# Optimization experiments

Hardware: AMD Instinct MI355X
Metric: run time of the kernel (lower is better)

## Reference

```python
import jax, jax.numpy as jnp
from jax import lax
import numpy as np

EPS = 1e-8
NUM_ROUTES = 1152  # 32 * 6 * 6
NUM_OBJ = 10
OBJ_DIM = 16
PC_CAPS = 8
PC_CH = 32


def _squash(s, axis=-1):
    sq = jnp.sum(s * s, axis=axis, keepdims=True)
    return (sq / (1.0 + sq)) * s / jnp.sqrt(sq + EPS)


def setup_inputs() -> dict:
    key = jax.random.key(0)
    ks = jax.random.split(key, 12)
    B = 512
    image = jax.random.uniform(ks[0], (B, 1, 28, 28), dtype=jnp.float32)
    label = jax.random.randint(ks[1], (B,), 0, NUM_OBJ)
    conv_w = jax.random.normal(ks[2], (256, 1, 9, 9), dtype=jnp.float32) * 0.05
    conv_b = jnp.zeros((256,), jnp.float32)
    pc_w = jax.random.normal(ks[3], (PC_CAPS, PC_CH, 256, 9, 9), dtype=jnp.float32) * 0.02
    pc_b = jnp.zeros((PC_CAPS, PC_CH), jnp.float32)
    W_route = jax.random.normal(ks[4], (NUM_ROUTES, NUM_OBJ, OBJ_DIM, PC_CAPS), dtype=jnp.float32)
    dec_w1 = jax.random.normal(ks[5], (512, NUM_OBJ * OBJ_DIM), dtype=jnp.float32) * 0.05
    dec_b1 = jnp.zeros((512,), jnp.float32)
    dec_w2 = jax.random.normal(ks[6], (1024, 512), dtype=jnp.float32) * 0.05
    dec_b2 = jnp.zeros((1024,), jnp.float32)
    dec_w3 = jax.random.normal(ks[7], (784, 1024), dtype=jnp.float32) * 0.05
    dec_b3 = jnp.zeros((784,), jnp.float32)
    return {"image": image, "label": label, "conv_w": conv_w, "conv_b": conv_b,
            "pc_w": pc_w, "pc_b": pc_b, "W_route": W_route,
            "dec_w1": dec_w1, "dec_b1": dec_b1, "dec_w2": dec_w2, "dec_b2": dec_b2,
            "dec_w3": dec_w3, "dec_b3": dec_b3}


def reference(image, label, conv_w, conv_b, pc_w, pc_b, W_route,
              dec_w1, dec_b1, dec_w2, dec_b2, dec_w3, dec_b3):
    B = image.shape[0]
    # ConvEncoder: [B,1,28,28] -> [B,256,20,20]
    x = lax.conv_general_dilated(image, conv_w, (1, 1), 'VALID',
                                 dimension_numbers=('NCHW', 'OIHW', 'NCHW'))
    x = jax.nn.relu(x + conv_b[None, :, None, None])
    # PrimaryCaps: 8 parallel convs fused into one conv with 8*32 out channels
    pw = pc_w.reshape(PC_CAPS * PC_CH, 256, 9, 9)
    u = lax.conv_general_dilated(x, pw, (2, 2), 'VALID',
                                 dimension_numbers=('NCHW', 'OIHW', 'NCHW'))
    u = u + pc_b.reshape(-1)[None, :, None, None]  # [B,256,6,6] == stack dim=1 of [B,8,32,6,6]
    # faithful torch .view: [B,8,32,6,6] row-major -> [B,1152,8]
    u = u.reshape(B, NUM_ROUTES, PC_CAPS)
    u = _squash(u, axis=-1)
    # ObjectCaps dynamic routing
    # u_hat[b,r,j,o] = sum_c W[r,j,o,c] * u[b,r,c]
    u_hat = jnp.einsum('rjoc,brc->brjo', W_route, u)  # [B,1152,10,16]
    b_ij = jnp.zeros((B, NUM_ROUTES, NUM_OBJ), u_hat.dtype)
    v = None
    for it in range(3):
        c_ij = jax.nn.softmax(b_ij, axis=2)                  # softmax over capsules j
        s_j = jnp.einsum('brj,brjo->bjo', c_ij, u_hat)       # [B,10,16]
        v = _squash(s_j, axis=-1)
        if it < 2:
            b_ij = b_ij + jnp.einsum('brjo,bjo->brj', u_hat, v)
    obj_vectors = v[..., None]  # [B,10,16,1]
    # safe_norm over dim=2, squeeze(-1)
    y_prob = jnp.sqrt(jnp.sum(v * v, axis=-1) + EPS)  # [B,10]
    # Decoder: mask by label one-hot, MLP to reconstruction
    mask = jax.nn.one_hot(label, NUM_OBJ, dtype=v.dtype)
    masked = (v * mask[:, :, None]).reshape(B, NUM_OBJ * OBJ_DIM)
    h = jax.nn.relu(masked @ dec_w1.T + dec_b1)
    h = jax.nn.relu(h @ dec_w2.T + dec_b2)
    recon = jax.nn.sigmoid(h @ dec_w3.T + dec_b3).reshape(B, 1, 28, 28)
    return obj_vectors, recon, y_prob
```

## Files before the change

kernel.cpp:

```cpp
#include <hip/hip_runtime.h>
#include <hip/hip_bf16.h>

#define EPSF 1e-8f

typedef __attribute__((ext_vector_type(8))) short short8v;
typedef __attribute__((ext_vector_type(4))) float float4v;

static __device__ __forceinline__ unsigned short f2bf_bits(float x)
{
    return __builtin_bit_cast(unsigned short, __float2bfloat16(x));
}

__global__ __launch_bounds__(256) void k_bw2(const float* __restrict__ pw,
                                             __hip_bfloat16* __restrict__ Bw2)
{
    const int oc = blockIdx.x;
    const int t = threadIdx.x;
    __shared__ unsigned short wl[20736];
    for (int i = t; i < 20736; i += 256)
        wl[i] = f2bf_bits(pw[(size_t)oc * 20736 + i]);
    __syncthreads();
    const int r16 = oc & 15, nt = (oc >> 4) & 3, wcq = oc >> 6;
    for (int e = t; e < 2592; e += 256) {
        const int kidx = e >> 5, icc = (e >> 2) & 7, slot = e & 3;
        short8v v;
        #pragma unroll
        for (int i = 0; i < 8; ++i)
            v[i] = (short)wl[(icc * 32 + slot * 8 + i) * 81 + kidx];
        const int chunk = ((kidx * 8 + icc) * 4 + wcq) * 4 + nt;
        *(short8v*)(Bw2 + (size_t)chunk * 512 + (slot * 16 + r16) * 8) = v;
    }
}

__global__ __launch_bounds__(256) void k_conv1(const float* __restrict__ img,
                                               const float* __restrict__ cw,
                                               const float* __restrict__ cb,
                                               __hip_bfloat16* __restrict__ xt)
{
    const int b = blockIdx.x;
    const int c = threadIdx.x;
    __shared__ float simg[784];
    for (int i = c; i < 784; i += 256) simg[i] = img[b * 784 + i];
    float wreg[81];
    const float* wp = cw + c * 81;
    #pragma unroll
    for (int k = 0; k < 81; ++k) wreg[k] = wp[k];
    const float bias = cb[c];
    __syncthreads();

    const int icc = c >> 5, slot = (c >> 3) & 3, ic8 = c & 7;
    char* xbase = (char*)xt + ((size_t)b * 8 + icc) * 25600;

    for (int h = 0; h < 20; ++h) {
        for (int wg = 0; wg < 5; ++wg) {
            float acc[4] = {bias, bias, bias, bias};
            #pragma unroll
            for (int ky = 0; ky < 9; ++ky) {
                const float* rp = &simg[(h + ky) * 28 + wg * 4];
                float v[12];
                #pragma unroll
                for (int i = 0; i < 12; ++i) v[i] = rp[i];
                #pragma unroll
                for (int kx = 0; kx < 9; ++kx) {
                    const float wv = wreg[ky * 9 + kx];
                    #pragma unroll
                    for (int i = 0; i < 4; ++i)
                        acc[i] = fmaf(v[kx + i], wv, acc[i]);
                }
            }
            #pragma unroll
            for (int i = 0; i < 4; ++i) {
                int w = wg * 4 + i;
                float av = fmaxf(acc[i], 0.f);
                int pos = h * 20 + (w & 1) * 10 + (w >> 1);
                int off = pos * 64 + ((slot ^ ((pos >> 1) & 3)) << 4) + ic8 * 2;
                *(unsigned short*)(xbase + off) = f2bf_bits(av);
            }
        }
    }
}

__device__ __forceinline__ void stage_x(const __hip_bfloat16* __restrict__ xt,
                                        char* dst, int b0, int icc, int t)
{
    const __hip_bfloat16* base0 = xt + ((size_t)(b0    ) * 8 + icc) * 12800;
    const __hip_bfloat16* base1 = xt + ((size_t)(b0 + 1) * 8 + icc) * 12800;
    #pragma unroll
    for (int k = 0; k < 6; ++k) {
        const int unit = t + k * 512;
        const __hip_bfloat16* gp = (unit < 1600) ? (base0 + unit * 8)
                                                 : (base1 + (unit - 1600) * 8);
        __builtin_amdgcn_global_load_lds(
            (const __attribute__((address_space(1))) unsigned int*)gp,
            (__attribute__((address_space(3))) unsigned int*)(dst + unit * 16),
            16, 0, 0);
    }
    if (t < 128) {
        const int unit = 3072 + t;
        const __hip_bfloat16* gp = base1 + (unit - 1600) * 8;
        __builtin_amdgcn_global_load_lds(
            (const __attribute__((address_space(1))) unsigned int*)gp,
            (__attribute__((address_space(3))) unsigned int*)(dst + unit * 16),
            16, 0, 0);
    }
}

__global__ __launch_bounds__(512) void k_conv2(const __hip_bfloat16* __restrict__ xt,
                                               const __hip_bfloat16* __restrict__ Bw2,
                                               const float* __restrict__ pcb,
                                               float* __restrict__ u)
{
    const int b0 = blockIdx.x * 2;
    const int t = threadIdx.x;
    const int lane = t & 63, wid = t >> 6;
    const int wr = wid >> 2, wc = wid & 3;
    const int r16 = lane & 15, slot = lane >> 4;

    __shared__ alignas(16) char xs[2][51200];

    int lc[3];
    #pragma unroll
    for (int mt = 0; mt < 3; ++mt) {
        int hw = mt * 16 + r16;
        if (hw >= 36) hw = 0;
        int h = hw / 6, w = hw - h * 6;
        lc[mt] = 40 * h + w;
    }

    float4v acc[3][4];
    #pragma unroll
    for (int mt = 0; mt < 3; ++mt)
        #pragma unroll
        for (int nt = 0; nt < 4; ++nt)
            acc[mt][nt] = (float4v){0.f, 0.f, 0.f, 0.f};

    stage_x(xt, xs[0], b0, 0, t);
    __syncthreads();

    for (int icc = 0; icc < 8; ++icc) {
        const int cur = icc & 1;
        if (icc < 7) stage_x(xt, xs[cur ^ 1], b0, icc + 1, t);

        const char* xw = xs[cur] + wr * 25600;
        const size_t bK = ((size_t)icc * 4 + wc) * 2048 + lane * 8;

        #pragma unroll 3
        for (int kidx = 0; kidx < 81; ++kidx) {
            int ky = kidx / 9, kx = kidx - ky * 9;
            int scalK = 20 * ky + 10 * (kx & 1) + (kx >> 1);
            short8v a[3];
            #pragma unroll
            for (int mt = 0; mt < 3; ++mt) {
                int pos = lc[mt] + scalK;
                int off = pos * 64 + (((slot ^ (pos >> 1)) & 3) << 4);
                a[mt] = *(const short8v*)(xw + off);
            }
            const __hip_bfloat16* bp = Bw2 + (size_t)kidx * 65536 + bK;
            short8v bv[4];
            #pragma unroll
            for (int nt = 0; nt < 4; ++nt)
                bv[nt] = *(const short8v*)(bp + nt * 512);
            #pragma unroll
            for (int mt = 0; mt < 3; ++mt)
                #pragma unroll
                for (int nt = 0; nt < 4; ++nt)
                    acc[mt][nt] = __builtin_amdgcn_mfma_f32_16x16x32_bf16(a[mt], bv[nt], acc[mt][nt], 0, 0, 0);
        }
        __syncthreads();
    }

    const int b = b0 + wr;
    #pragma unroll
    for (int mt = 0; mt < 3; ++mt) {
        int hwb = mt * 16 + slot * 4;
        if (hwb < 36) {
            #pragma unroll
            for (int nt = 0; nt < 4; ++nt) {
                int oc = wc * 64 + nt * 16 + r16;
                float pb = pcb[oc];
                float4v v = acc[mt][nt];
                v.x += pb; v.y += pb; v.z += pb; v.w += pb;
                *(float4v*)(u + (size_t)b * 9216 + oc * 36 + hwb) = v;
            }
        }
    }
}

__global__ void k_squash_u(float* __restrict__ u, int ngroups)
{
    int g = blockIdx.x * blockDim.x + threadIdx.x;
    if (g >= ngroups) return;
    float4v* p = (float4v*)(u + (size_t)g * 8);
    float4v a = p[0], c = p[1];
    float sq = a.x * a.x + a.y * a.y + a.z * a.z + a.w * a.w
             + c.x * c.x + c.y * c.y + c.z * c.z + c.w * c.w;
    float scale = (sq / (1.f + sq)) / sqrtf(sq + EPSF);
    a *= scale; c *= scale;
    p[0] = a; p[1] = c;
}

__global__ __launch_bounds__(256, 2) void k_route3(const float* __restrict__ u,
                                                   const float* __restrict__ W,
                                                   const float* __restrict__ vsum,
                                                   float* __restrict__ spart, int iter)
{
    const int bid = blockIdx.x;
    const int rc = bid % 144;
    const int bc = bid / 144;
    const int r0 = rc * 8;
    const int b0 = bc * 64;
    const int t = threadIdx.x;
    const int oq = t & 3;
    const int img = t >> 2;
    const int b = b0 + img;

    __shared__ alignas(16) float Wl[10240];
    __shared__ alignas(16) float ul[64 * 68];

    #pragma unroll
    for (int k = 0; k < 10; ++k) {
        int e = t + k * 256;
        int rr = e / 320, rest = e - rr * 320;
        float4v val = *(const float4v*)(W + (size_t)(r0 + rr) * 1280 + rest * 4);
        int es = e ^ ((e >> 3) & 3);
        *(float4v*)(Wl + es * 4) = val;
    }
    #pragma unroll
    for (int k = 0; k < 4; ++k) {
        int e = t + k * 256;
        int im = e >> 4, f4 = e & 15;
        float4v val = *(const float4v*)(u + (size_t)(b0 + im) * 9216 + rc * 64 + f4 * 4);
        *(float4v*)(ul + im * 68 + f4 * 4) = val;
    }
    __syncthreads();

    float4v vv[10];
    if (iter > 0) {
        #pragma unroll
        for (int j = 0; j < 10; ++j)
            vv[j] = *(const float4v*)(vsum + (size_t)b * 160 + j * 16 + oq * 4);
    }

    float4v acc[10];
    #pragma unroll
    for (int j = 0; j < 10; ++j) acc[j] = (float4v){0.f, 0.f, 0.f, 0.f};

    const float* up = ul + img * 68;

    for (int r = 0; r < 8; ++r) {
        float4v u0 = *(const float4v*)(up + r * 8);
        float4v u1 = *(const float4v*)(up + r * 8 + 4);
        float4v uh[10];
        #pragma unroll
        for (int j = 0; j < 10; ++j) {
            #pragma unroll
            for (int oo = 0; oo < 4; ++oo) {
                int un = r * 320 + j * 32 + oq * 8 + oo * 2;
                int i0 = un ^ oq;
                int i1 = i0 ^ 1;
                float4v wlo = *(const float4v*)(Wl + i0 * 4);
                float4v whi = *(const float4v*)(Wl + i1 * 4);
                uh[j][oo] = wlo.x * u0.x + wlo.y * u0.y + wlo.z * u0.z + wlo.w * u0.w
                          + whi.x * u1.x + whi.y * u1.y + whi.z * u1.z + whi.w * u1.w;
            }
        }
        if (iter > 0) {
            float q[10];
            #pragma unroll
            for (int j = 0; j < 10; ++j) {
                float qp = uh[j].x * vv[j].x + uh[j].y * vv[j].y
                         + uh[j].z * vv[j].z + uh[j].w * vv[j].w;
                qp += __shfl_xor(qp, 1);
                qp += __shfl_xor(qp, 2);
                q[j] = qp;
            }
            float mx = q[0];
            #pragma unroll
            for (int j = 1; j < 10; ++j) mx = fmaxf(mx, q[j]);
            float ssum = 0.f;
            float c[10];
            #pragma unroll
            for (int j = 0; j < 10; ++j) { c[j] = __expf(q[j] - mx); ssum += c[j]; }
            float inv = 1.f / ssum;
            #pragma unroll
            for (int j = 0; j < 10; ++j) acc[j] += (c[j] * inv) * uh[j];
        } else {
            #pragma unroll
            for (int j = 0; j < 10; ++j) acc[j] += 0.1f * uh[j];
        }
    }

    float* dst = spart + ((size_t)rc * 512 + b) * 160 + oq * 4;
    #pragma unroll
    for (int j = 0; j < 10; ++j)
        *(float4v*)(dst + j * 16) = acc[j];
}

__global__ void k_finish(const float* __restrict__ spart, float* __restrict__ vsum,
                         const int* __restrict__ label, float* __restrict__ obj,
                         float* __restrict__ yprob, float* __restrict__ masked, int iter)
{
    const int b = blockIdx.x, t = threadIdx.x;
    if (t < 160) {
        const float* sp = spart + (size_t)b * 160 + t;
        float sv = 0.f;
        #pragma unroll 8
        for (int rc = 0; rc < 144; ++rc)
            sv += sp[(size_t)rc * 81920];
        float sq = sv * sv;
        sq += __shfl_xor(sq, 1); sq += __shfl_xor(sq, 2);
        sq += __shfl_xor(sq, 4); sq += __shfl_xor(sq, 8);
        float v = sv * (sq / (1.f + sq)) / sqrtf(sq + EPSF);
        float pv = (iter > 0) ? vsum[b * 160 + t] : 0.f;
        vsum[b * 160 + t] = pv + v;
        if (iter == 2) {
            obj[b * 160 + t] = v;
            float vv = v * v;
            vv += __shfl_xor(vv, 1); vv += __shfl_xor(vv, 2);
            vv += __shfl_xor(vv, 4); vv += __shfl_xor(vv, 8);
            int j = t >> 4;
            if ((t & 15) == 0) yprob[b * 10 + j] = sqrtf(vv + EPSF);
            masked[b * 160 + t] = (label[b] == j) ? v : 0.f;
        }
    }
}

__global__ void k_mlp(const float* __restrict__ A, const float* __restrict__ Wt,
                      const float* __restrict__ bias, float* __restrict__ C,
                      int N, int K, int act)
{
    const int m0 = blockIdx.x * 32;
    const int n0 = blockIdx.y * 32;
    const int t  = threadIdx.x;
    const int tn = t & 31, tg = t >> 5;
    __shared__ float As[32][33];
    __shared__ float Ws[32][33];
    float acc[4] = {0.f, 0.f, 0.f, 0.f};
    for (int k0 = 0; k0 < K; k0 += 32) {
        __syncthreads();
        for (int idx = t; idx < 1024; idx += 256) {
            int rr = idx >> 5, kk = idx & 31;
            As[rr][kk] = A[(size_t)(m0 + rr) * K + k0 + kk];
            int n = n0 + rr;
            Ws[rr][kk] = (n < N) ? Wt[(size_t)n * K + k0 + kk] : 0.f;
        }
        __syncthreads();
        #pragma unroll 8
        for (int kk = 0; kk < 32; ++kk) {
            float bv = Ws[tn][kk];
            #pragma unroll
            for (int i = 0; i < 4; ++i)
                acc[i] += As[tg * 4 + i][kk] * bv;
        }
    }
    int n = n0 + tn;
    if (n < N) {
        float bs = bias[n];
        #pragma unroll
        for (int i = 0; i < 4; ++i) {
            float vv = acc[i] + bs;
            vv = (act == 0) ? fmaxf(vv, 0.f) : 1.f / (1.f + expf(-vv));
            C[(size_t)(m0 + tg * 4 + i) * N + n] = vv;
        }
    }
}

extern "C" void kernel_launch(void* const* d_in, const int* in_sizes, int n_in,
                              void* d_out, int out_size, void* d_ws, size_t ws_size,
                              hipStream_t stream)
{
    const float* image  = (const float*)d_in[0];
    const int*   label  = (const int*)  d_in[1];
    const float* conv_w = (const float*)d_in[2];
    const float* conv_b = (const float*)d_in[3];
    const float* pc_w   = (const float*)d_in[4];
    const float* pc_b   = (const float*)d_in[5];
    const float* Wrt    = (const float*)d_in[6];
    const float* dw1 = (const float*)d_in[7];
    const float* db1 = (const float*)d_in[8];
    const float* dw2 = (const float*)d_in[9];
    const float* db2 = (const float*)d_in[10];
    const float* dw3 = (const float*)d_in[11];
    const float* db3 = (const float*)d_in[12];
    float* out = (float*)d_out;

    char* p = (char*)d_ws;
    __hip_bfloat16* xt  = (__hip_bfloat16*)p; p += 104857600;
    float* u      = (float*)p; p += 18874368;
    __hip_bfloat16* Bw2 = (__hip_bfloat16*)p; p += 10616832;
    float* vsum   = (float*)p; p += 327680;
    float* masked = (float*)p; p += 327680;
    float* h1     = (float*)p; p += 1048576;
    float* h2     = (float*)p; p += 2097152;

    float* spart = (float*)xt;

    float* obj   = out;
    float* recon = out + 81920;
    float* yprob = out + 483328;

    k_bw2<<<256, 256, 0, stream>>>(pc_w, Bw2);
    k_conv1<<<512, 256, 0, stream>>>(image, conv_w, conv_b, xt);
    k_conv2<<<256, 512, 0, stream>>>(xt, Bw2, pc_b, u);
    k_squash_u<<<2304, 256, 0, stream>>>(u, 589824);
    for (int it = 0; it < 3; ++it) {
        k_route3<<<1152, 256, 0, stream>>>(u, Wrt, vsum, spart, it);
        k_finish<<<512, 192, 0, stream>>>(spart, vsum, label, obj, yprob, masked, it);
    }
    k_mlp<<<dim3(16, 16), 256, 0, stream>>>(masked, dw1, db1, h1, 512, 160, 0);
    k_mlp<<<dim3(16, 32), 256, 0, stream>>>(h1, dw2, db2, h2, 1024, 512, 0);
    k_mlp<<<dim3(16, 25), 256, 0, stream>>>(h2, dw3, db3, recon, 784, 1024, 1);
}
```

Before: 757.3 us.

## Pad conv2 input tile layout to avoid XOR swizzle and simplify LDS addressing

Changes the bf16 activation layout written by conv1 and staged into shared memory by conv2: instead of an XOR-swizzled 64-byte-per-position layout, each 16-byte channel slot gets its own padded plane (row stride 23, slot stride 7312) so bank conflicts are avoided by padding. The conv2 inner loop is restructured into ky/kx nests with fully unrolled kx and constant LDS offsets, removing per-iteration swizzle arithmetic, and launch bounds pin one block per CU. The cost is a larger LDS footprint (two 58 KB buffers) and slightly more global traffic from the padding.

```diff
diff --git a/kernel.cpp b/kernel.cpp
--- a/kernel.cpp
+++ b/kernel.cpp
@@ -5,6 +5,9 @@
 
 typedef __attribute__((ext_vector_type(8))) short short8v;
 typedef __attribute__((ext_vector_type(4))) float float4v;
+
+#define XREG 29248
+#define XSLOT 7312
 
 static __device__ __forceinline__ unsigned short f2bf_bits(float x)
 {
@@ -49,7 +52,7 @@
     __syncthreads();
 
     const int icc = c >> 5, slot = (c >> 3) & 3, ic8 = c & 7;
-    char* xbase = (char*)xt + ((size_t)b * 8 + icc) * 25600;
+    char* xbase = (char*)xt + ((size_t)b * 8 + icc) * XREG + slot * XSLOT + ic8 * 2;
 
     for (int h = 0; h < 20; ++h) {
         for (int wg = 0; wg < 5; ++wg) {
@@ -72,9 +75,8 @@
             for (int i = 0; i < 4; ++i) {
                 int w = wg * 4 + i;
                 float av = fmaxf(acc[i], 0.f);
-                int pos = h * 20 + (w & 1) * 10 + (w >> 1);
-                int off = pos * 64 + ((slot ^ ((pos >> 1) & 3)) << 4) + ic8 * 2;
-                *(unsigned short*)(xbase + off) = f2bf_bits(av);
+                int pos = 23 * h + 10 * (w & 1) + (w >> 1);
+                *(unsigned short*)(xbase + pos * 16) = f2bf_bits(av);
             }
         }
     }
@@ -83,21 +85,21 @@
 __device__ __forceinline__ void stage_x(const __hip_bfloat16* __restrict__ xt,
                                         char* dst, int b0, int icc, int t)
 {
-    const __hip_bfloat16* base0 = xt + ((size_t)(b0    ) * 8 + icc) * 12800;
-    const __hip_bfloat16* base1 = xt + ((size_t)(b0 + 1) * 8 + icc) * 12800;
-    #pragma unroll
-    for (int k = 0; k < 6; ++k) {
+    const char* base0 = (const char*)xt + ((size_t)(b0    ) * 8 + icc) * XREG;
+    const char* base1 = (const char*)xt + ((size_t)(b0 + 1) * 8 + icc) * XREG;
+    #pragma unroll
+    for (int k = 0; k < 7; ++k) {
         const int unit = t + k * 512;
-        const __hip_bfloat16* gp = (unit < 1600) ? (base0 + unit * 8)
-                                                 : (base1 + (unit - 1600) * 8);
+        const char* gp = (unit < 1828) ? (base0 + unit * 16)
+                                       : (base1 + (unit - 1828) * 16);
         __builtin_amdgcn_global_load_lds(
             (const __attribute__((address_space(1))) unsigned int*)gp,
             (__attribute__((address_space(3))) unsigned int*)(dst + unit * 16),
             16, 0, 0);
     }
-    if (t < 128) {
-        const int unit = 3072 + t;
-        const __hip_bfloat16* gp = base1 + (unit - 1600) * 8;
+    if (t < 72) {
+        const int unit = 3584 + t;
+        const char* gp = base1 + (unit - 1828) * 16;
         __builtin_amdgcn_global_load_lds(
             (const __attribute__((address_space(1))) unsigned int*)gp,
             (__attribute__((address_space(3))) unsigned int*)(dst + unit * 16),
@@ -105,10 +107,10 @@
     }
 }
 
-__global__ __launch_bounds__(512) void k_conv2(const __hip_bfloat16* __restrict__ xt,
-                                               const __hip_bfloat16* __restrict__ Bw2,
-                                               const float* __restrict__ pcb,
-                                               float* __restrict__ u)
+__global__ __launch_bounds__(512, 1) void k_conv2(const __hip_bfloat16* __restrict__ xt,
+                                                  const __hip_bfloat16* __restrict__ Bw2,
+                                                  const float* __restrict__ pcb,
+                                                  float* __restrict__ u)
 {
     const int b0 = blockIdx.x * 2;
     const int t = threadIdx.x;
@@ -116,7 +118,7 @@
     const int wr = wid >> 2, wc = wid & 3;
     const int r16 = lane & 15, slot = lane >> 4;
 
-    __shared__ alignas(16) char xs[2][51200];
+    __shared__ alignas(16) char xs[2][58496];
 
     int lc[3];
     #pragma unroll
@@ -124,8 +126,9 @@
         int hw = mt * 16 + r16;
         if (hw >= 36) hw = 0;
         int h = hw / 6, w = hw - h * 6;
-        lc[mt] = 40 * h + w;
-    }
+        lc[mt] = 46 * h + w;
+    }
+    const int abase0 = wr * XREG + slot * XSLOT;
 
     float4v acc[3][4];
     #pragma unroll
@@ -141,30 +144,38 @@
         const int cur = icc & 1;
         if (icc < 7) stage_x(xt, xs[cur ^ 1], b0, icc + 1, t);
 
-        const char* xw = xs[cur] + wr * 25600;
-        const size_t bK = ((size_t)icc * 4 + wc) * 2048 + lane * 8;
-
-        #pragma unroll 3
-        for (int kidx = 0; kidx < 81; ++kidx) {
-            int ky = kidx / 9, kx = kidx - ky * 9;
-            int scalK = 20 * ky + 10 * (kx & 1) + (kx >> 1);
-            short8v a[3];
-            #pragma unroll
-            for (int mt = 0; mt < 3; ++mt) {
-                int pos = lc[mt] + scalK;
-                int off = pos * 64 + (((slot ^ (pos >> 1)) & 3) << 4);
-                a[mt] = *(const short8v*)(xw + off);
-            }
-            const __hip_bfloat16* bp = Bw2 + (size_t)kidx * 65536 + bK;
-            short8v bv[4];
-            #pragma unroll
-            for (int nt = 0; nt < 4; ++nt)
-                bv[nt] = *(const short8v*)(bp + nt * 512);
-            #pragma unroll
-            for (int mt = 0; mt < 3; ++mt)
-                #pragma unroll
-                for (int nt = 0; nt < 4; ++nt)
-                    acc[mt][nt] = __builtin_amdgcn_mfma_f32_16x16x32_bf16(a[mt], bv[nt], acc[mt][nt], 0, 0, 0);
+        const char* xw = xs[cur];
+        const __hip_bfloat16* bp = Bw2 + ((size_t)icc * 4 + wc) * 2048 + lane * 8;
+
+        for (int ky = 0; ky < 9; ++ky) {
+            const char* ap0 = xw + abase0 + (lc[0] + 23 * ky) * 16;
+            const char* ap1 = xw + abase0 + (lc[1] + 23 * ky) * 16;
+            const char* ap2 = xw + abase0 + (lc[2] + 23 * ky) * 16;
+            const __hip_bfloat16* bk = bp + (size_t)ky * 9 * 65536;
+            #pragma unroll
+            for (int kx = 0; kx < 9; ++kx) {
+                const int C = (10 * (kx & 1) + (kx >> 1)) * 16;
+                short8v a0 = *(const short8v*)(ap0 + C);
+                short8v a1 = *(const short8v*)(ap1 + C);
+                short8v a2 = *(const short8v*)(ap2 + C);
+                const __hip_bfloat16* bq = bk + (size_t)kx * 65536;
+                short8v bv0 = *(const short8v*)(bq);
+                short8v bv1 = *(const short8v*)(bq + 512);
+                short8v bv2 = *(const short8v*)(bq + 1024);
+                short8v bv3 = *(const short8v*)(bq + 1536);
+                acc[0][0] = __builtin_amdgcn_mfma_f32_16x16x32_bf16(a0, bv0, acc[0][0], 0, 0, 0);
+                acc[0][1] = __builtin_amdgcn_mfma_f32_16x16x32_bf16(a0, bv1, acc[0][1], 0, 0, 0);
+                acc[0][2] = __builtin_amdgcn_mfma_f32_16x16x32_bf16(a0, bv2, acc[0][2], 0, 0, 0);
+                acc[0][3] = __builtin_amdgcn_mfma_f32_16x16x32_bf16(a0, bv3, acc[0][3], 0, 0, 0);
+                acc[1][0] = __builtin_amdgcn_mfma_f32_16x16x32_bf16(a1, bv0, acc[1][0], 0, 0, 0);
+                acc[1][1] = __builtin_amdgcn_mfma_f32_16x16x32_bf16(a1, bv1, acc[1][1], 0, 0, 0);
+                acc[1][2] = __builtin_amdgcn_mfma_f32_16x16x32_bf16(a1, bv2, acc[1][2], 0, 0, 0);
+                acc[1][3] = __builtin_amdgcn_mfma_f32_16x16x32_bf16(a1, bv3, acc[1][3], 0, 0, 0);
+                acc[2][0] = __builtin_amdgcn_mfma_f32_16x16x32_bf16(a2, bv0, acc[2][0], 0, 0, 0);
+                acc[2][1] = __builtin_amdgcn_mfma_f32_16x16x32_bf16(a2, bv1, acc[2][1], 0, 0, 0);
+                acc[2][2] = __builtin_amdgcn_mfma_f32_16x16x32_bf16(a2, bv2, acc[2][2], 0, 0, 0);
+                acc[2][3] = __builtin_amdgcn_mfma_f32_16x16x32_bf16(a2, bv3, acc[2][3], 0, 0, 0);
+            }
         }
         __syncthreads();
     }
@@ -385,7 +396,7 @@
     float* out = (float*)d_out;
 
     char* p = (char*)d_ws;
-    __hip_bfloat16* xt  = (__hip_bfloat16*)p; p += 104857600;
+    __hip_bfloat16* xt  = (__hip_bfloat16*)p; p += (size_t)512 * 8 * XREG;
     float* u      = (float*)p; p += 18874368;
     __hip_bfloat16* Bw2 = (__hip_bfloat16*)p; p += 10616832;
     float* vsum   = (float*)p; p += 327680;
```

Result: slower. 786.3 us (+3.8%).
